# Performance work log

Hardware: AMD Instinct MI355X
Metric: run time of the kernel (lower is better)

## Reference

```python
import jax, jax.numpy as jnp
import numpy as np

TAU = 0.2          # rank_temperature
LAM = 8.0          # lambda_value
TOPO = 0.5         # topology_influence
LEN_C = 0.01       # edge_length_coeff
SP_C = 0.001       # edge_sparsity_coeff
B, M, D = 4096, 256, 256


def _pairwise_sq(a, b):
    # [Na, D] x [Nb, D] -> [Na, Nb] squared L2 distances
    sq = (jnp.sum(a * a, -1)[:, None] - 2.0 * (a @ b.T)
          + jnp.sum(b * b, -1)[None, :])
    return jnp.maximum(sq, 0.0)


def setup_inputs() -> dict:
    key = jax.random.key(0)
    k1, k2, k3 = jax.random.split(key, 3)
    data = jax.random.normal(k1, (B, D), dtype=jnp.float32)
    weights = jax.random.uniform(k2, (M, D), dtype=jnp.float32)
    # edge logits initialized near edge_init_logit (-2.0) with small noise
    edge_logits = -2.0 + 0.1 * jax.random.normal(k3, (M, M), dtype=jnp.float32)
    return {"data": data, "weights": weights, "edge_logits": edge_logits}


def reference(data, weights, edge_logits):
    m = weights.shape[0]
    eye = jnp.eye(m, dtype=data.dtype)

    # distances: [B, M], l2
    distances = jnp.sqrt(_pairwise_sq(data, weights))

    # soft rank: [B, M]; pairwise sigmoid with zeroed diagonal
    diff = (distances[:, :, None] - distances[:, None, :]) / TAU  # [B, M, M]
    prob_greater = jax.nn.sigmoid(diff) * (1.0 - eye)[None]
    soft_rank = 1.0 + jnp.sum(prob_greater, axis=-1)

    # exponential neighborhood weighting
    neighborhood = jnp.exp(-(soft_rank - 1.0) / LAM)

    # symmetric edge probabilities with zero diagonal
    logits = 0.5 * (edge_logits + edge_logits.T)
    edge_prob = jax.nn.sigmoid(logits) * (1.0 - eye)

    degree = jnp.sum(edge_prob, axis=1) / float(m - 1)
    neighborhood = neighborhood * (1.0 + TOPO * degree[None, :])

    data_term = jnp.mean(neighborhood * distances)

    proto_dist = _pairwise_sq(weights, weights)  # sq_l2
    weighted_len = jnp.sum(edge_prob * proto_dist) / (jnp.sum(edge_prob) + 1e-8)
    sparsity = jnp.mean(edge_prob)

    loss = data_term + LEN_C * weighted_len + SP_C * sparsity
    return loss
```

## Files before the change

kernel.cpp:

```cpp
#include <hip/hip_runtime.h>
#include <math.h>

#define B_N 4096
#define M_N 256
#define D_N 256
#define ROWS 2
#define GRID_MAIN (B_N / ROWS)
#define NSLOT 64
#define BLK_PER_SLOT (GRID_MAIN / NSLOT)

constexpr float TAU_   = 0.2f;
constexpr float LAM_   = 8.0f;
constexpr float TOPO_  = 0.5f;
constexpr float LEN_C_ = 0.01f;
constexpr float SP_C_  = 0.001f;
constexpr float LOG2E_ = 1.44269504088896340736f;
constexpr float KSC    = LOG2E_ / TAU_;
constexpr float KL     = LOG2E_ / LAM_;
constexpr float C0_    = 133.0f;


__device__ __forceinline__ float wave_reduce_sum(float v) {
#pragma unroll
  for (int off = 1; off < 64; off <<= 1) v += __shfl_xor(v, off, 64);
  return v;
}

__device__ __forceinline__ void rank_quad(float iv, float iv2, float4 q,
                                          float& s) {
  float ta = fmaf(q.x, iv, 1.0f);
  float da = fmaf(q.y, iv2, ta);
  float na = ta + 1.0f;
  float tb = fmaf(q.z, iv, 1.0f);
  float db = fmaf(q.w, iv2, tb);
  float nb = tb + 1.0f;
  float d4 = da * db;
  float n4 = fmaf(na, db, nb * da);
  s = fmaf(n4, __builtin_amdgcn_rcpf(d4), s);
}

__global__ __launch_bounds__(256) void k_prep(const float* __restrict__ w,
                                              const float* __restrict__ E,
                                              float* __restrict__ ws) {
  int tid = threadIdx.x;
  if (blockIdx.x < M_N) {
    float* wT = ws + 8192;
    int j = blockIdx.x, d = tid;
    float v = w[j * D_N + d];
    wT[d * M_N + j] = v;
    float s = wave_reduce_sum(v * v);
    __shared__ float red[4];
    if ((d & 63) == 0) red[d >> 6] = s;
    if (j == 0) {
      if (d < 16) ws[d] = 0.0f;
      if (d < NSLOT) {
        ws[2048 + 16 * d] = 0.0f;
        ((unsigned*)ws)[4096 + 16 * d] = 0u;
      }
    }
    __syncthreads();
    if (d == 0) ws[512 + j] = red[0] + red[1] + red[2] + red[3];
  } else {
    int j = blockIdx.x - M_N;
    int k = tid;
    __shared__ __align__(16) float sp[M_N];
    __shared__ float redp[4], redt[4];

    float l = 0.5f * (E[j * M_N + k] + E[k * M_N + j]);
    float p = __builtin_amdgcn_rcpf(1.0f + __builtin_amdgcn_exp2f(-l * LOG2E_));
    if (k == j) p = 0.0f;
    sp[k] = p;

    float spw = wave_reduce_sum(p);
    if ((k & 63) == 0) redp[k >> 6] = spw;
    __syncthreads();
    float tp = redp[0] + redp[1] + redp[2] + redp[3];

    float A = 0.0f, Bv = 0.0f;
    const float4* sp4 = (const float4*)sp;
    const float* wb = w + tid;
#pragma unroll 4
    for (int k0 = 0; k0 < M_N / 4; k0++) {
      float4 pq = sp4[k0];
      const float* wr = wb + (size_t)(4 * k0) * D_N;
      float w0 = wr[0], w1 = wr[D_N], w2 = wr[2 * D_N], w3 = wr[3 * D_N];
      A  = fmaf(pq.x, w0 * w0, A); Bv = fmaf(pq.x, w0, Bv);
      A  = fmaf(pq.y, w1 * w1, A); Bv = fmaf(pq.y, w1, Bv);
      A  = fmaf(pq.z, w2 * w2, A); Bv = fmaf(pq.z, w2, Bv);
      A  = fmaf(pq.w, w3 * w3, A); Bv = fmaf(pq.w, w3, Bv);
    }

    float wj = w[j * D_N + tid];
    float v  = fmaf(tp, wj * wj, fmaf(-2.0f * wj, Bv, A));
    float sv = wave_reduce_sum(v);
    if ((k & 63) == 0) redt[k >> 6] = sv;
    __syncthreads();
    if (k == 0) {
      float tw = redt[0] + redt[1] + redt[2] + redt[3];
      ws[16 + j]   = tp * (1.0f / (float)(M_N - 1));
      ws[1024 + j] = tp;
      ws[1280 + j] = tw;
    }
  }
}

__global__ __launch_bounds__(256, 4) void k_main(const float* __restrict__ data,
                                                 float* __restrict__ ws,
                                                 float* __restrict__ out) {
  const float* wT     = ws + 8192;
  const float* wnorm  = ws + 512;
  const float* degree = ws + 16;
  float* S_slot  = ws + 2048;
  unsigned* cnt1 = (unsigned*)ws + 4096;
  unsigned* cnt2 = (unsigned*)ws + 4;

  __shared__ __align__(16) float ew[ROWS][M_N];
  __shared__ __align__(16) float ewp[ROWS][M_N];
  __shared__ float rednrm[ROWS][4];
  __shared__ float snrm[ROWS];
  __shared__ float redf[4], redp[4], redw[4];
  __shared__ int isLast;

  const int tid  = threadIdx.x;
  const int wv_  = tid >> 6;
  const int lane = tid & 63;
  const int b0   = blockIdx.x * ROWS;

#pragma unroll
  for (int r = 0; r < ROWS; r++) {
    float x = data[(size_t)(b0 + r) * D_N + tid];
    float s = wave_reduce_sum(x * x);
    if (lane == 0) rednrm[r][wv_] = s;
  }
  __syncthreads();
  if (tid < ROWS)
    snrm[tid] = rednrm[tid][0] + rednrm[tid][1] + rednrm[tid][2] + rednrm[tid][3];

  const float4* x0 = (const float4*)(data + (size_t)(b0 + 0) * D_N);
  const float4* x1 = (const float4*)(data + (size_t)(b0 + 1) * D_N);
  const float* pw = wT + tid;

  float a0 = 0.f, a1 = 0.f;
  float wreg[2][16];
#pragma unroll
  for (int i = 0; i < 16; i++) wreg[0][i] = pw[(size_t)i * M_N];

#pragma unroll
  for (int g = 0; g < 16; g++) {
    const int cur = g & 1, nxt = cur ^ 1;
    if (g < 15) {
#pragma unroll
      for (int i = 0; i < 16; i++)
        wreg[nxt][i] = pw[(size_t)((g + 1) * 16 + i) * M_N];
    }
#pragma unroll
    for (int i4 = 0; i4 < 4; i4++) {
      int d4 = 4 * g + i4;
      float4 xa = x0[d4], xb = x1[d4];
      float w0 = wreg[cur][4 * i4 + 0], w1 = wreg[cur][4 * i4 + 1];
      float w2 = wreg[cur][4 * i4 + 2], w3 = wreg[cur][4 * i4 + 3];
      a0 = fmaf(xa.x, w0, a0); a0 = fmaf(xa.y, w1, a0);
      a0 = fmaf(xa.z, w2, a0); a0 = fmaf(xa.w, w3, a0);
      a1 = fmaf(xb.x, w0, a1); a1 = fmaf(xb.y, w1, a1);
      a1 = fmaf(xb.z, w2, a1); a1 = fmaf(xb.w, w3, a1);
    }
  }
  __syncthreads();

  float wn = wnorm[tid];
  float acc[ROWS] = {a0, a1};
  float dist[ROWS], iv[ROWS], iv2[ROWS];
#pragma unroll
  for (int r = 0; r < ROWS; r++) {
    float sq = snrm[r] - 2.0f * acc[r] + wn;
    dist[r] = sqrtf(fmaxf(sq, 0.0f));
    float sc = dist[r] * KSC;
    ew[r][tid] = __builtin_amdgcn_exp2f(sc - C0_);
    iv[r]      = __builtin_amdgcn_exp2f(C0_ - sc);
    iv2[r]     = iv[r] * iv[r];
  }
  __syncthreads();

  {
    int p  = tid;
    int r  = p >> 7, idx = p & 127;
    float ea = ew[r][2 * idx], eb = ew[r][2 * idx + 1];
    ewp[r][2 * idx]     = ea + eb;
    ewp[r][2 * idx + 1] = ea * eb;
  }
  __syncthreads();

  float fj = 1.0f + TOPO_ * degree[tid];
  float tl = 0.0f;
#pragma unroll
  for (int r = 0; r < ROWS; r++) {
    float s = 0.0f;
    const float4* q4 = (const float4*)(&ewp[r][0]);
    float ivr = iv[r], iv2r = iv2[r];
#pragma unroll 8
    for (int k4 = 0; k4 < M_N / 4; k4++) {
      float4 q = q4[k4];
      rank_quad(ivr, iv2r, q, s);
    }
    float nb = __builtin_amdgcn_exp2f((0.5f - s) * KL);
    tl = fmaf(nb * dist[r], fj, tl);
  }

  float bs = wave_reduce_sum(tl);
  if (lane == 0) redf[wv_] = bs;
  __syncthreads();
  if (tid == 0) {
    float tot = redf[0] + redf[1] + redf[2] + redf[3];
    int slot = (int)(blockIdx.x & (NSLOT - 1));
    float old = atomicAdd(&S_slot[16 * slot], tot);
    asm volatile("" : "+v"(old));
    int last = 0;
    unsigned t1 = atomicAdd(&cnt1[16 * slot], 1u);
    if (t1 == (unsigned)(BLK_PER_SLOT - 1)) {
      unsigned t2 = atomicAdd(cnt2, 1u);
      last = (t2 == (unsigned)(NSLOT - 1)) ? 1 : 0;
    }
    isLast = last;
  }
  __syncthreads();

  if (isLast) {
    float p  = ws[1024 + tid];
    float wd = ws[1280 + tid];
    float rp = wave_reduce_sum(p);
    float rw = wave_reduce_sum(wd);
    if (lane == 0) { redp[wv_] = rp; redw[wv_] = rw; }
    float sd = 0.0f;
    if (wv_ == 0) {
      float v = atomicAdd(&S_slot[16 * lane], 0.0f);
      sd = wave_reduce_sum(v);
    }
    __syncthreads();
    if (tid == 0) {
      float Sp   = redp[0] + redp[1] + redp[2] + redp[3];
      float Swpd = redw[0] + redw[1] + redw[2] + redw[3];
      float data_term = sd * (1.0f / ((float)B_N * (float)M_N));
      float wl = Swpd / (Sp + 1e-8f);
      float sparsity = Sp * (1.0f / ((float)M_N * (float)M_N));
      out[0] = data_term + LEN_C_ * wl + SP_C_ * sparsity;
    }
  }
}

extern "C" void kernel_launch(void* const* d_in, const int* in_sizes, int n_in,
                              void* d_out, int out_size, void* d_ws, size_t ws_size,
                              hipStream_t stream) {
  const float* data = (const float*)d_in[0];
  const float* w    = (const float*)d_in[1];
  const float* E    = (const float*)d_in[2];
  float* ws = (float*)d_ws;

  k_prep<<<2 * M_N, 256, 0, stream>>>(w, E, ws);
  k_main<<<GRID_MAIN, 256, 0, stream>>>(data, ws, (float*)d_out);
}
```

Measured before the change: 101.0 us.

## Process eight data rows per block and pair exponentials via lane shuffles

Raises rows per block from 2 to 8, so each loaded column of the transposed weights is reused across eight distance dot products and the grid is four times smaller. Row norms are now computed with float4 loads, one row per wave. The intermediate ew shared array and its extra barrier are replaced by a lane-pair shuffle that writes the sum and product of neighbouring exponentials directly. In exchange, register pressure rises from the eight accumulators and per-row arrays, and the grid has fewer blocks to fill the GPU.

```diff
diff --git a/kernel.cpp b/kernel.cpp
--- a/kernel.cpp
+++ b/kernel.cpp
@@ -4,7 +4,7 @@
 #define B_N 4096
 #define M_N 256
 #define D_N 256
-#define ROWS 2
+#define ROWS 8
 #define GRID_MAIN (B_N / ROWS)
 #define NSLOT 64
 #define BLK_PER_SLOT (GRID_MAIN / NSLOT)
@@ -114,9 +114,7 @@
   unsigned* cnt1 = (unsigned*)ws + 4096;
   unsigned* cnt2 = (unsigned*)ws + 4;
 
-  __shared__ __align__(16) float ew[ROWS][M_N];
   __shared__ __align__(16) float ewp[ROWS][M_N];
-  __shared__ float rednrm[ROWS][4];
   __shared__ float snrm[ROWS];
   __shared__ float redf[4], redp[4], redw[4];
   __shared__ int isLast;
@@ -127,20 +125,23 @@
   const int b0   = blockIdx.x * ROWS;
 
 #pragma unroll
-  for (int r = 0; r < ROWS; r++) {
-    float x = data[(size_t)(b0 + r) * D_N + tid];
-    float s = wave_reduce_sum(x * x);
-    if (lane == 0) rednrm[r][wv_] = s;
-  }
-  __syncthreads();
-  if (tid < ROWS)
-    snrm[tid] = rednrm[tid][0] + rednrm[tid][1] + rednrm[tid][2] + rednrm[tid][3];
-
-  const float4* x0 = (const float4*)(data + (size_t)(b0 + 0) * D_N);
-  const float4* x1 = (const float4*)(data + (size_t)(b0 + 1) * D_N);
+  for (int h = 0; h < 2; h++) {
+    int r = wv_ + 4 * h;
+    float4 xv = ((const float4*)(data + (size_t)(b0 + r) * D_N))[lane];
+    float s = wave_reduce_sum(fmaf(xv.x, xv.x, fmaf(xv.y, xv.y,
+                              fmaf(xv.z, xv.z, xv.w * xv.w))));
+    if (lane == 0) snrm[r] = s;
+  }
+
+  const float4* xp[ROWS];
+#pragma unroll
+  for (int r = 0; r < ROWS; r++)
+    xp[r] = (const float4*)(data + (size_t)(b0 + r) * D_N);
   const float* pw = wT + tid;
 
-  float a0 = 0.f, a1 = 0.f;
+  float acc[ROWS];
+#pragma unroll
+  for (int r = 0; r < ROWS; r++) acc[r] = 0.0f;
   float wreg[2][16];
 #pragma unroll
   for (int i = 0; i < 16; i++) wreg[0][i] = pw[(size_t)i * M_N];
@@ -156,37 +157,33 @@
 #pragma unroll
     for (int i4 = 0; i4 < 4; i4++) {
       int d4 = 4 * g + i4;
-      float4 xa = x0[d4], xb = x1[d4];
       float w0 = wreg[cur][4 * i4 + 0], w1 = wreg[cur][4 * i4 + 1];
       float w2 = wreg[cur][4 * i4 + 2], w3 = wreg[cur][4 * i4 + 3];
-      a0 = fmaf(xa.x, w0, a0); a0 = fmaf(xa.y, w1, a0);
-      a0 = fmaf(xa.z, w2, a0); a0 = fmaf(xa.w, w3, a0);
-      a1 = fmaf(xb.x, w0, a1); a1 = fmaf(xb.y, w1, a1);
-      a1 = fmaf(xb.z, w2, a1); a1 = fmaf(xb.w, w3, a1);
+#pragma unroll
+      for (int r = 0; r < ROWS; r++) {
+        float4 xa = xp[r][d4];
+        acc[r] = fmaf(xa.x, w0, acc[r]); acc[r] = fmaf(xa.y, w1, acc[r]);
+        acc[r] = fmaf(xa.z, w2, acc[r]); acc[r] = fmaf(xa.w, w3, acc[r]);
+      }
     }
   }
   __syncthreads();
 
   float wn = wnorm[tid];
-  float acc[ROWS] = {a0, a1};
   float dist[ROWS], iv[ROWS], iv2[ROWS];
 #pragma unroll
   for (int r = 0; r < ROWS; r++) {
     float sq = snrm[r] - 2.0f * acc[r] + wn;
     dist[r] = sqrtf(fmaxf(sq, 0.0f));
     float sc = dist[r] * KSC;
-    ew[r][tid] = __builtin_amdgcn_exp2f(sc - C0_);
-    iv[r]      = __builtin_amdgcn_exp2f(C0_ - sc);
-    iv2[r]     = iv[r] * iv[r];
-  }
-  __syncthreads();
-
-  {
-    int p  = tid;
-    int r  = p >> 7, idx = p & 127;
-    float ea = ew[r][2 * idx], eb = ew[r][2 * idx + 1];
-    ewp[r][2 * idx]     = ea + eb;
-    ewp[r][2 * idx + 1] = ea * eb;
+    float ev = __builtin_amdgcn_exp2f(sc - C0_);
+    iv[r]    = __builtin_amdgcn_exp2f(C0_ - sc);
+    iv2[r]   = iv[r] * iv[r];
+    float en = __shfl_xor(ev, 1, 64);
+    if ((tid & 1) == 0) {
+      float2 o = {ev + en, ev * en};
+      *(float2*)&ewp[r][tid] = o;
+    }
   }
   __syncthreads();
 
```

Measured after the change: 107.2 us. 1.06x slower.
